# Kernel optimization log

Hardware: AMD Instinct MI355X
Metric: run time of the kernel (lower is better)

## Reference

```python
import jax, jax.numpy as jnp
import numpy as np

D_MODEL = 1024
NUM_HEADS = 16
DEPTH = D_MODEL // NUM_HEADS


def setup_inputs() -> dict:
    key = jax.random.key(0)
    k_x, k_wqkv, k_bqkv, k_wp, k_bp = jax.random.split(key, 5)
    B, N = 2, 2048
    x = jax.random.normal(k_x, (B, N, D_MODEL), dtype=jnp.float32)
    scale = 1.0 / np.sqrt(D_MODEL)
    Wqkv = jax.random.normal(k_wqkv, (D_MODEL, 3 * D_MODEL), dtype=jnp.float32) * scale
    bqkv = jnp.zeros((3 * D_MODEL,), dtype=jnp.float32)
    Wproj = jax.random.normal(k_wp, (D_MODEL, D_MODEL), dtype=jnp.float32) * scale
    bproj = jnp.zeros((D_MODEL,), dtype=jnp.float32)
    return {"x": x, "Wqkv": Wqkv, "bqkv": bqkv, "Wproj": Wproj, "bproj": bproj}


def reference(x, Wqkv, bqkv, Wproj, bproj):
    B, N, C = x.shape
    # QKV projection; original layout: [B, N, H, depth, 3] -> transpose to [B, 3, H, N, depth]
    qkv = x @ Wqkv + bqkv                      # [B, N, 3C]
    qkv = qkv.reshape(B, N, NUM_HEADS, DEPTH, 3)
    qkv = jnp.transpose(qkv, (0, 4, 2, 1, 3))  # [B, 3, H, N, depth]
    q, k, v = qkv[:, 0], qkv[:, 1], qkv[:, 2]  # each [B, H, N, depth]
    # scaled dot-product attention (full N x N scores, as in the original)
    scale = 1.0 / jnp.sqrt(jnp.asarray(DEPTH, dtype=x.dtype))
    attn = jnp.einsum("bhnd,bhmd->bhnm", q, k) * scale
    attn = jax.nn.softmax(attn.astype(jnp.float32), axis=-1).astype(x.dtype)
    out = jnp.einsum("bhnm,bhmd->bhnd", attn, v)  # [B, H, N, depth]
    out = jnp.transpose(out, (0, 2, 1, 3)).reshape(B, N, C)
    return out @ Wproj + bproj
```

## Files before the change

### kernel.cpp

```cpp
#include <hip/hip_runtime.h>
#include <stdint.h>

#define D_MODEL 1024
#define NHEADS  16
#define DEPTH   64
#define BATCH   2
#define SEQ     2048
#define M_TOK   (BATCH*SEQ)

typedef __attribute__((ext_vector_type(8)))  short short8;
typedef __attribute__((ext_vector_type(4)))  float f32x4;
typedef __attribute__((ext_vector_type(16))) float f32x16;
typedef __attribute__((ext_vector_type(4)))  unsigned int uint4v;

#if defined(__has_builtin)
#if __has_builtin(__builtin_amdgcn_exp2f)
#define EXP2(x) __builtin_amdgcn_exp2f(x)
#endif
#endif
#ifndef EXP2
#define EXP2(x) exp2f(x)
#endif

__device__ __forceinline__ unsigned short f2bf(float f) {
  unsigned int u = __float_as_uint(f);
  u += 0x7fffu + ((u >> 16) & 1u);
  return (unsigned short)(u >> 16);
}

__device__ __forceinline__ unsigned int cvt_pk_bf16(float lo, float hi) {
  unsigned int r;
  asm("v_cvt_pk_bf16_f32 %0, %1, %2" : "=v"(r) : "v"(lo), "v"(hi));
  return r;
}

__device__ __forceinline__ void gload_lds16(const unsigned short* g, unsigned short* l) {
  __builtin_amdgcn_global_load_lds((const __attribute__((address_space(1))) void*)g,
                                   (__attribute__((address_space(3))) void*)l, 16, 0, 0);
}

__global__ void mha_prep(const float* __restrict__ x, const float* __restrict__ Wqkv,
                         const float* __restrict__ Wproj,
                         unsigned short* __restrict__ xb,
                         unsigned short* __restrict__ wqkT,
                         unsigned short* __restrict__ wvT,
                         unsigned short* __restrict__ wpT) {
  __shared__ float tile[32][33];
  int id = blockIdx.x, t = threadIdx.x;
  if (id < 2048) {
    int i = (id * 256 + t) * 8;
    float4 a = *(const float4*)(x + i);
    float4 b = *(const float4*)(x + i + 4);
    uint4 r;
    r.x = (unsigned)f2bf(a.x) | ((unsigned)f2bf(a.y) << 16);
    r.y = (unsigned)f2bf(a.z) | ((unsigned)f2bf(a.w) << 16);
    r.z = (unsigned)f2bf(b.x) | ((unsigned)f2bf(b.y) << 16);
    r.w = (unsigned)f2bf(b.z) | ((unsigned)f2bf(b.w) << 16);
    *(uint4*)(xb + i) = r;
  } else if (id < 5120) {
    int b = id - 2048;
    int c0 = (b % 96) * 32, k0 = (b / 96) * 32;
    int tx = t & 31, ty = t >> 5;
    for (int i = ty; i < 32; i += 8)
      tile[i][tx] = Wqkv[(size_t)(k0 + i) * 3072 + c0 + tx];
    __syncthreads();
    for (int i = ty; i < 32; i += 8) {
      int c = c0 + i;
      int hd = c / 3;
      int s = c - hd * 3;
      unsigned short v = f2bf(tile[tx][i]);
      if (s < 2) wqkT[(size_t)(s * 1024 + hd) * 1024 + k0 + tx] = v;
      else       wvT [(size_t)hd * 1024 + k0 + tx] = v;
    }
  } else {
    int b = id - 5120;
    int c0 = (b & 31) * 32, k0 = (b >> 5) * 32;
    int tx = t & 31, ty = t >> 5;
    for (int i = ty; i < 32; i += 8)
      tile[i][tx] = Wproj[(size_t)(k0 + i) * 1024 + c0 + tx];
    __syncthreads();
    for (int i = ty; i < 32; i += 8)
      wpT[(size_t)(c0 + i) * 1024 + k0 + tx] = f2bf(tile[tx][i]);
  }
}

__global__ __launch_bounds__(256, 3) void mha_gemm_qkv(
    const unsigned short* __restrict__ xb,
    const unsigned short* __restrict__ wqkT,
    const unsigned short* __restrict__ wvT,
    const float* __restrict__ bias,
    unsigned short* __restrict__ Qb,
    unsigned short* __restrict__ Kb,
    unsigned short* __restrict__ Vtb)
{
  __shared__ __align__(16) unsigned short As[128 * 64];
  __shared__ __align__(16) unsigned short Bs[128 * 64];
  const int K = 1024;
  int id = blockIdx.x;
  bool m0 = id < 512;
  int bx, by, bz = 0;
  const unsigned short *A, *Bt;
  if (m0) {
    int xcd = id & 7, idx = id >> 3;
    by = xcd * 4 + (idx >> 4);
    bx = idx & 15;
    A = xb; Bt = wqkT;
  } else {
    int b2 = id - 512;
    bx = b2 & 15; by = (b2 >> 4) & 7; bz = b2 >> 7;
    A = wvT; Bt = xb + (size_t)bz * SEQ * D_MODEL;
  }
  int t = threadIdx.x;
  int wv = t >> 6, lane = t & 63;
  int l15 = lane & 15, l4 = lane >> 4;
  int wr = wv >> 1, wc = wv & 1;
  int blkM = by * 128, blkN = bx * 128;

  f32x4 acc[4][4];
  for (int m = 0; m < 4; m++) for (int n = 0; n < 4; n++) acc[m][n] = (f32x4){0.f,0.f,0.f,0.f};

  for (int kt = 0; kt < K; kt += 64) {
    #pragma unroll
    for (int i = 0; i < 4; i++) {
      int e = i * 256 + t;
      int row = e >> 3;
      int sc = ((e & 7) ^ (row & 7)) * 8;
      gload_lds16(A  + (size_t)(blkM + row) * K + kt + sc, As + e * 8);
      gload_lds16(Bt + (size_t)(blkN + row) * K + kt + sc, Bs + e * 8);
    }
    __syncthreads();
    #pragma unroll
    for (int kk = 0; kk < 2; kk++) {
      int gp = ((kk * 4 + l4) ^ (l15 & 7)) * 8;
      short8 af[4], bf[4];
      #pragma unroll
      for (int m = 0; m < 4; m++)
        af[m] = *(const short8*)&As[(wr * 64 + m * 16 + l15) * 64 + gp];
      #pragma unroll
      for (int n = 0; n < 4; n++)
        bf[n] = *(const short8*)&Bs[(wc * 64 + n * 16 + l15) * 64 + gp];
      #pragma unroll
      for (int m = 0; m < 4; m++)
        #pragma unroll
        for (int n = 0; n < 4; n++)
          acc[m][n] = __builtin_amdgcn_mfma_f32_16x16x32_bf16(af[m], bf[n], acc[m][n], 0, 0, 0);
    }
    __syncthreads();
  }

  int row0 = blkM + wr * 64;
  int col0 = blkN + wc * 64;
  #pragma unroll
  for (int m = 0; m < 4; m++) {
    #pragma unroll
    for (int n = 0; n < 4; n++) {
      int colb = col0 + n * 16 + l15;
      #pragma unroll
      for (int j = 0; j < 4; j++) {
        int row = row0 + m * 16 + l4 * 4 + j;
        float v = acc[m][n][j];
        if (m0) {
          int s = colb >> 10, hd = colb & 1023;
          v += bias[hd * 3 + s];
          if (s == 0) v *= 0.18033688011112042f;
          size_t idx = ((size_t)((row >> 11) * NHEADS + (hd >> 6)) * SEQ + (row & 2047)) * DEPTH + (hd & 63);
          (s == 0 ? Qb : Kb)[idx] = f2bf(v);
        } else {
          v += bias[row * 3 + 2];
          Vtb[((size_t)(bz * 1024 + row)) * SEQ + colb] = f2bf(v);
        }
      }
    }
  }
}

__global__ __launch_bounds__(256, 3) void mha_gemm_proj(
    const unsigned short* __restrict__ A,
    const unsigned short* __restrict__ Bt,
    const float* __restrict__ bias,
    float* __restrict__ out_f)
{
  __shared__ __align__(16) unsigned short As[128 * 64];
  __shared__ __align__(16) unsigned short Bs[64 * 64];
  const int K = 1024;
  int id = blockIdx.x;
  int xcd = id & 7, idx = id >> 3;
  int by = xcd * 4 + (idx >> 4);
  int bx = idx & 15;
  int t = threadIdx.x;
  int wv = t >> 6, lane = t & 63;
  int l15 = lane & 15, l4 = lane >> 4;
  int wr = wv >> 1, wc = wv & 1;
  int blkM = by * 128, blkN = bx * 64;

  f32x4 acc[4][2];
  for (int m = 0; m < 4; m++) for (int n = 0; n < 2; n++) acc[m][n] = (f32x4){0.f,0.f,0.f,0.f};

  for (int kt = 0; kt < K; kt += 64) {
    #pragma unroll
    for (int i = 0; i < 4; i++) {
      int e = i * 256 + t;
      int row = e >> 3;
      int sc = ((e & 7) ^ (row & 7)) * 8;
      gload_lds16(A + (size_t)(blkM + row) * K + kt + sc, As + e * 8);
    }
    #pragma unroll
    for (int i = 0; i < 2; i++) {
      int e = i * 256 + t;
      int row = e >> 3;
      int sc = ((e & 7) ^ (row & 7)) * 8;
      gload_lds16(Bt + (size_t)(blkN + row) * K + kt + sc, Bs + e * 8);
    }
    __syncthreads();
    #pragma unroll
    for (int kk = 0; kk < 2; kk++) {
      int gp = ((kk * 4 + l4) ^ (l15 & 7)) * 8;
      short8 af[4], bf[2];
      #pragma unroll
      for (int m = 0; m < 4; m++)
        af[m] = *(const short8*)&As[(wr * 64 + m * 16 + l15) * 64 + gp];
      #pragma unroll
      for (int n = 0; n < 2; n++)
        bf[n] = *(const short8*)&Bs[(wc * 32 + n * 16 + l15) * 64 + gp];
      #pragma unroll
      for (int m = 0; m < 4; m++)
        #pragma unroll
        for (int n = 0; n < 2; n++)
          acc[m][n] = __builtin_amdgcn_mfma_f32_16x16x32_bf16(af[m], bf[n], acc[m][n], 0, 0, 0);
    }
    __syncthreads();
  }

  int row0 = blkM + wr * 64;
  int col0 = blkN + wc * 32;
  #pragma unroll
  for (int m = 0; m < 4; m++) {
    #pragma unroll
    for (int n = 0; n < 2; n++) {
      int colb = col0 + n * 16 + l15;
      #pragma unroll
      for (int j = 0; j < 4; j++) {
        int row = row0 + m * 16 + l4 * 4 + j;
        out_f[(size_t)row * D_MODEL + colb] = acc[m][n][j] + bias[colb];
      }
    }
  }
}

__global__ __launch_bounds__(512, 2) void mha_attn(
    const unsigned short* __restrict__ Q,
    const unsigned short* __restrict__ Kb,
    const unsigned short* __restrict__ Vt,
    unsigned short* __restrict__ O)
{
  const int N = SEQ;
  const int NIT = N / 128;
  int id = blockIdx.x;
  int bh    = (id & 7) * 4 + ((id >> 7) & 3);
  int qtile = (id >> 3) & 15;
  int t = threadIdx.x, wv = t >> 6, lane = t & 63;
  int l31 = lane & 31, hi = lane >> 5;
  int kh = wv & 1, qh = wv >> 1;

  __shared__ __align__(16) unsigned short SMEM[2 * 16384];

  const unsigned short* Kbh = Kb + (size_t)bh * N * DEPTH;
  const unsigned short* Vbh = Vt + (size_t)bh * DEPTH * N;

  int qrow = qtile * 128 + qh * 32 + l31;
  const unsigned short* Qp = Q + ((size_t)bh * N + qrow) * DEPTH + hi * 8;
  short8 qf[4];
  #pragma unroll
  for (int c = 0; c < 4; c++) qf[c] = *(const short8*)(Qp + c * 16);

  int krow = t >> 3;
  int ksc  = ((t & 7) ^ (krow & 7)) * 8;
  const unsigned short* kst = Kbh + (size_t)krow * DEPTH + ksc;
  int vrow = t >> 4;
  int vg   = t & 15;
  int vsc  = ((vg ^ (vrow & 7))) * 8;
  const unsigned short* vst = Vbh + (size_t)vrow * N + vsc;

  int rbK0 = (kh * 64 + l31) * 64;
  int rbV0 = l31 * 128, rbV1 = rbV0 + 4096;
  int goQK[4], goPV[4];
  #pragma unroll
  for (int c = 0; c < 4; c++) goQK[c] = ((c * 2 + hi) ^ (l31 & 7)) * 8;
  #pragma unroll
  for (int i = 0; i < 4; i++) {
    int g = i >> 1, lc = i & 1;
    goPV[i] = ((kh * 8 + g * 4 + lc * 2 + hi) ^ (l31 & 7)) * 8;
  }

  short8 ones;
  #pragma unroll
  for (int i = 0; i < 8; i++) ones[i] = (short)0x3F80;

  f32x16 o0, o1, lsacc, zc;
  #pragma unroll
  for (int i = 0; i < 16; i++) { o0[i] = 0.f; o1[i] = 0.f; lsacc[i] = 0.f; zc[i] = 0.f; }

  gload_lds16(kst,                       SMEM + t * 8);
  gload_lds16(kst + 4096,                SMEM + 4096 + t * 8);
  gload_lds16(vst,                       SMEM + 8192 + t * 8);
  gload_lds16(vst + (size_t)32 * N,      SMEM + 12288 + t * 8);
  asm volatile("s_waitcnt vmcnt(0)" ::: "memory");
  __builtin_amdgcn_sched_barrier(0);
  __builtin_amdgcn_s_barrier();
  __builtin_amdgcn_sched_barrier(0);

#define BODY(BUF, IT)                                                                     \
  do {                                                                                    \
    if ((IT) + 1 < NIT) {                                                                 \
      unsigned short* nb = SMEM + ((BUF) ^ 1) * 16384;                                    \
      const unsigned short* kn = kst + (size_t)((IT) + 1) * 8192;                         \
      const unsigned short* vn = vst + ((IT) + 1) * 128;                                  \
      gload_lds16(kn,                  nb + t * 8);                                       \
      gload_lds16(kn + 4096,           nb + 4096 + t * 8);                                \
      gload_lds16(vn,                  nb + 8192 + t * 8);                                \
      gload_lds16(vn + (size_t)32 * N, nb + 12288 + t * 8);                               \
    }                                                                                     \
    {                                                                                     \
      const unsigned short* Kc = SMEM + (BUF) * 16384;                                    \
      const unsigned short* Vc = Kc + 8192;                                               \
      _Pragma("unroll") for (int g = 0; g < 2; g++) {                                     \
        __builtin_amdgcn_s_setprio(1);                                                    \
        short8 ka0 = *(const short8*)&Kc[rbK0 + g * 2048 + goQK[0]];                      \
        f32x16 s = __builtin_amdgcn_mfma_f32_32x32x16_bf16(ka0, qf[0], zc, 0, 0, 0);      \
        _Pragma("unroll") for (int c = 1; c < 4; c++) {                                   \
          short8 ka = *(const short8*)&Kc[rbK0 + g * 2048 + goQK[c]];                     \
          s = __builtin_amdgcn_mfma_f32_32x32x16_bf16(ka, qf[c], s, 0, 0, 0);             \
        }                                                                                 \
        __builtin_amdgcn_s_setprio(0);                                                    \
        float p[16];                                                                      \
        _Pragma("unroll") for (int r = 0; r < 16; r++) p[r] = EXP2(s[r]);                 \
        _Pragma("unroll") for (int lc = 0; lc < 2; lc++) {                                \
          unsigned int X0 = cvt_pk_bf16(p[8*lc+0], p[8*lc+1]);                            \
          unsigned int X1 = cvt_pk_bf16(p[8*lc+2], p[8*lc+3]);                            \
          unsigned int X2 = cvt_pk_bf16(p[8*lc+4], p[8*lc+5]);                            \
          unsigned int X3 = cvt_pk_bf16(p[8*lc+6], p[8*lc+7]);                            \
          auto r02 = __builtin_amdgcn_permlane32_swap(X0, X2, false, false);              \
          auto r13 = __builtin_amdgcn_permlane32_swap(X1, X3, false, false);              \
          uint4v wvec; wvec[0] = r02[0]; wvec[1] = r13[0]; wvec[2] = r02[1]; wvec[3] = r13[1]; \
          short8 bfrag = __builtin_bit_cast(short8, wvec);                                \
          short8 va = *(const short8*)&Vc[rbV0 + goPV[g * 2 + lc]];                       \
          short8 vb = *(const short8*)&Vc[rbV1 + goPV[g * 2 + lc]];                       \
          __builtin_amdgcn_s_setprio(1);                                                  \
          o0 = __builtin_amdgcn_mfma_f32_32x32x16_bf16(va, bfrag, o0, 0, 0, 0);           \
          o1 = __builtin_amdgcn_mfma_f32_32x32x16_bf16(vb, bfrag, o1, 0, 0, 0);           \
          lsacc = __builtin_amdgcn_mfma_f32_32x32x16_bf16(ones, bfrag, lsacc, 0, 0, 0);   \
          __builtin_amdgcn_s_setprio(0);                                                  \
        }                                                                                 \
      }                                                                                   \
    }                                                                                     \
    if ((IT) + 1 < NIT) {                                                                 \
      asm volatile("s_waitcnt vmcnt(0)" ::: "memory");                                    \
      __builtin_amdgcn_sched_barrier(0);                                                  \
      __builtin_amdgcn_s_barrier();                                                       \
      __builtin_amdgcn_sched_barrier(0);                                                  \
    }                                                                                     \
  } while (0)

  for (int it2 = 0; it2 < NIT; it2 += 2) {
    BODY(0, it2);
    BODY(1, it2 + 1);
  }
#undef BODY

  float ls = lsacc[0];

  __syncthreads();
  float* cmb = (float*)SMEM;
  if (kh == 1) {
    float* c0 = cmb + (qh * 64 + lane) * 33;
    #pragma unroll
    for (int i = 0; i < 16; i++) { c0[i] = o0[i]; c0[16 + i] = o1[i]; }
    c0[32] = ls;
  }
  __syncthreads();
  if (kh == 0) {
    const float* c0 = cmb + (qh * 64 + lane) * 33;
    #pragma unroll
    for (int i = 0; i < 16; i++) { o0[i] += c0[i]; o1[i] += c0[16 + i]; }
    float rl = 1.0f / (ls + c0[32]);

    int b = bh >> 4, h = bh & 15;
    unsigned short* Op = O + ((size_t)b * N + qrow) * D_MODEL + h * DEPTH;
    #pragma unroll
    for (int gq = 0; gq < 4; gq++) {
      #pragma unroll
      for (int rp = 0; rp < 2; rp++) {
        int reg = gq * 4 + rp * 2;
        int d = gq * 8 + hi * 4 + rp * 2;
        *(unsigned int*)(Op + d)      = cvt_pk_bf16(o0[reg] * rl, o0[reg + 1] * rl);
        *(unsigned int*)(Op + 32 + d) = cvt_pk_bf16(o1[reg] * rl, o1[reg + 1] * rl);
      }
    }
  }
}

extern "C" void kernel_launch(void* const* d_in, const int* in_sizes, int n_in,
                              void* d_out, int out_size, void* d_ws, size_t ws_size,
                              hipStream_t stream) {
  const float* x     = (const float*)d_in[0];
  const float* Wqkv  = (const float*)d_in[1];
  const float* bqkv  = (const float*)d_in[2];
  const float* Wproj = (const float*)d_in[3];
  const float* bproj = (const float*)d_in[4];
  float* out = (float*)d_out;

  char* w = (char*)d_ws;
  unsigned short* xb    = (unsigned short*)(w);
  unsigned short* wqkT  = (unsigned short*)(w + 8388608);
  unsigned short* wvT   = (unsigned short*)(w + 8388608 + 4194304);
  unsigned short* wpT   = (unsigned short*)(w + 8388608 + 4194304 + 2097152);
  unsigned short* Qbuf  = (unsigned short*)(w + 16777216);
  unsigned short* Kbuf  = (unsigned short*)(w + 16777216 + 8388608);
  unsigned short* Vtb   = (unsigned short*)(w + 16777216 + 16777216);
  unsigned short* AOut  = (unsigned short*)(w + 16777216 + 25165824);

  mha_prep<<<6144, 256, 0, stream>>>(x, Wqkv, Wproj, xb, wqkT, wvT, wpT);
  mha_gemm_qkv<<<768, 256, 0, stream>>>(xb, wqkT, wvT, bqkv, Qbuf, Kbuf, Vtb);
  mha_attn<<<512, 512, 0, stream>>>(Qbuf, Kbuf, Vtb, AOut);
  mha_gemm_proj<<<512, 256, 0, stream>>>(AOut, wpT, bproj, out);
}
```

Before: 110.8 us.

## Read V fragments directly from global memory and swap MFMA operand roles in PV

V tiles are no longer staged through shared memory; each wave loads its V fragments straight from global memory into registers, which halves the LDS buffer size. The PV MFMAs swap operand order so P becomes the A operand, which transposes the output layout; the row-sum accumulator now holds per-row values and is combined across waves in full. The epilogue writes scalar bf16 stores per row instead of packed pairs. This trades LDS traffic and occupancy pressure for uncoalesced, latency-exposed global loads and narrower output stores.

```diff
diff --git a/kernel.cpp b/kernel.cpp
--- a/kernel.cpp
+++ b/kernel.cpp
@@ -262,13 +262,13 @@
   int l31 = lane & 31, hi = lane >> 5;
   int kh = wv & 1, qh = wv >> 1;
 
-  __shared__ __align__(16) unsigned short SMEM[2 * 16384];
+  __shared__ __align__(16) unsigned short SMEM[25600];
 
   const unsigned short* Kbh = Kb + (size_t)bh * N * DEPTH;
   const unsigned short* Vbh = Vt + (size_t)bh * DEPTH * N;
 
-  int qrow = qtile * 128 + qh * 32 + l31;
-  const unsigned short* Qp = Q + ((size_t)bh * N + qrow) * DEPTH + hi * 8;
+  int qbase = qtile * 128 + qh * 32;
+  const unsigned short* Qp = Q + ((size_t)bh * N + qbase + l31) * DEPTH + hi * 8;
   short8 qf[4];
   #pragma unroll
   for (int c = 0; c < 4; c++) qf[c] = *(const short8*)(Qp + c * 16);
@@ -276,21 +276,14 @@
   int krow = t >> 3;
   int ksc  = ((t & 7) ^ (krow & 7)) * 8;
   const unsigned short* kst = Kbh + (size_t)krow * DEPTH + ksc;
-  int vrow = t >> 4;
-  int vg   = t & 15;
-  int vsc  = ((vg ^ (vrow & 7))) * 8;
-  const unsigned short* vst = Vbh + (size_t)vrow * N + vsc;
-
-  int rbK0 = (kh * 64 + l31) * 64;
-  int rbV0 = l31 * 128, rbV1 = rbV0 + 4096;
-  int goQK[4], goPV[4];
+
+  int rbK = (kh * 64 + l31) * 64;
+  int goQK[4];
   #pragma unroll
   for (int c = 0; c < 4; c++) goQK[c] = ((c * 2 + hi) ^ (l31 & 7)) * 8;
-  #pragma unroll
-  for (int i = 0; i < 4; i++) {
-    int g = i >> 1, lc = i & 1;
-    goPV[i] = ((kh * 8 + g * 4 + lc * 2 + hi) ^ (l31 & 7)) * 8;
-  }
+
+  const unsigned short* vb0 = Vbh + (size_t)l31 * N + kh * 64 + hi * 8;
+  const unsigned short* vb1 = vb0 + (size_t)32 * N;
 
   short8 ones;
   #pragma unroll
@@ -300,10 +293,8 @@
   #pragma unroll
   for (int i = 0; i < 16; i++) { o0[i] = 0.f; o1[i] = 0.f; lsacc[i] = 0.f; zc[i] = 0.f; }
 
-  gload_lds16(kst,                       SMEM + t * 8);
-  gload_lds16(kst + 4096,                SMEM + 4096 + t * 8);
-  gload_lds16(vst,                       SMEM + 8192 + t * 8);
-  gload_lds16(vst + (size_t)32 * N,      SMEM + 12288 + t * 8);
+  gload_lds16(kst,        SMEM + t * 8);
+  gload_lds16(kst + 4096, SMEM + 4096 + t * 8);
   asm volatile("s_waitcnt vmcnt(0)" ::: "memory");
   __builtin_amdgcn_sched_barrier(0);
   __builtin_amdgcn_s_barrier();
@@ -312,23 +303,26 @@
 #define BODY(BUF, IT)                                                                     \
   do {                                                                                    \
     if ((IT) + 1 < NIT) {                                                                 \
-      unsigned short* nb = SMEM + ((BUF) ^ 1) * 16384;                                    \
+      unsigned short* nb = SMEM + ((BUF) ^ 1) * 8192;                                     \
       const unsigned short* kn = kst + (size_t)((IT) + 1) * 8192;                         \
-      const unsigned short* vn = vst + ((IT) + 1) * 128;                                  \
-      gload_lds16(kn,                  nb + t * 8);                                       \
-      gload_lds16(kn + 4096,           nb + 4096 + t * 8);                                \
-      gload_lds16(vn,                  nb + 8192 + t * 8);                                \
-      gload_lds16(vn + (size_t)32 * N, nb + 12288 + t * 8);                               \
+      gload_lds16(kn,        nb + t * 8);                                                 \
+      gload_lds16(kn + 4096, nb + 4096 + t * 8);                                          \
     }                                                                                     \
     {                                                                                     \
-      const unsigned short* Kc = SMEM + (BUF) * 16384;                                    \
-      const unsigned short* Vc = Kc + 8192;                                               \
+      const unsigned short* Kc = SMEM + (BUF) * 8192;                                     \
+      int kt0 = (IT) * 128;                                                               \
       _Pragma("unroll") for (int g = 0; g < 2; g++) {                                     \
+                            \
+        int voff = kt0 + g * 32;                                                          \
+        short8 vf00 = *(const short8*)(vb0 + voff);                                       \
+        short8 vf01 = *(const short8*)(vb1 + voff);                                       \
+        short8 vf10 = *(const short8*)(vb0 + voff + 16);                                  \
+        short8 vf11 = *(const short8*)(vb1 + voff + 16);                                  \
         __builtin_amdgcn_s_setprio(1);                                                    \
-        short8 ka0 = *(const short8*)&Kc[rbK0 + g * 2048 + goQK[0]];                      \
+        short8 ka0 = *(const short8*)&Kc[rbK + g * 2048 + goQK[0]];                       \
         f32x16 s = __builtin_amdgcn_mfma_f32_32x32x16_bf16(ka0, qf[0], zc, 0, 0, 0);      \
         _Pragma("unroll") for (int c = 1; c < 4; c++) {                                   \
-          short8 ka = *(const short8*)&Kc[rbK0 + g * 2048 + goQK[c]];                     \
+          short8 ka = *(const short8*)&Kc[rbK + g * 2048 + goQK[c]];                      \
           s = __builtin_amdgcn_mfma_f32_32x32x16_bf16(ka, qf[c], s, 0, 0, 0);             \
         }                                                                                 \
         __builtin_amdgcn_s_setprio(0);                                                    \
@@ -342,13 +336,11 @@
           auto r02 = __builtin_amdgcn_permlane32_swap(X0, X2, false, false);              \
           auto r13 = __builtin_amdgcn_permlane32_swap(X1, X3, false, false);              \
           uint4v wvec; wvec[0] = r02[0]; wvec[1] = r13[0]; wvec[2] = r02[1]; wvec[3] = r13[1]; \
-          short8 bfrag = __builtin_bit_cast(short8, wvec);                                \
-          short8 va = *(const short8*)&Vc[rbV0 + goPV[g * 2 + lc]];                       \
-          short8 vb = *(const short8*)&Vc[rbV1 + goPV[g * 2 + lc]];                       \
+          short8 pfrag = __builtin_bit_cast(short8, wvec);                                \
           __builtin_amdgcn_s_setprio(1);                                                  \
-          o0 = __builtin_amdgcn_mfma_f32_32x32x16_bf16(va, bfrag, o0, 0, 0, 0);           \
-          o1 = __builtin_amdgcn_mfma_f32_32x32x16_bf16(vb, bfrag, o1, 0, 0, 0);           \
-          lsacc = __builtin_amdgcn_mfma_f32_32x32x16_bf16(ones, bfrag, lsacc, 0, 0, 0);   \
+          o0 = __builtin_amdgcn_mfma_f32_32x32x16_bf16(pfrag, lc ? vf10 : vf00, o0, 0, 0, 0); \
+          o1 = __builtin_amdgcn_mfma_f32_32x32x16_bf16(pfrag, lc ? vf11 : vf01, o1, 0, 0, 0); \
+          lsacc = __builtin_amdgcn_mfma_f32_32x32x16_bf16(pfrag, ones, lsacc, 0, 0, 0);   \
           __builtin_amdgcn_s_setprio(0);                                                  \
         }                                                                                 \
       }                                                                                   \
@@ -367,34 +359,28 @@
   }
 #undef BODY
 
-  float ls = lsacc[0];
-
   __syncthreads();
   float* cmb = (float*)SMEM;
   if (kh == 1) {
-    float* c0 = cmb + (qh * 64 + lane) * 33;
-    #pragma unroll
-    for (int i = 0; i < 16; i++) { c0[i] = o0[i]; c0[16 + i] = o1[i]; }
-    c0[32] = ls;
+    float* c0 = cmb + (qh * 64 + lane) * 49;
+    #pragma unroll
+    for (int i = 0; i < 16; i++) { c0[i] = o0[i]; c0[16 + i] = o1[i]; c0[32 + i] = lsacc[i]; }
   }
   __syncthreads();
   if (kh == 0) {
-    const float* c0 = cmb + (qh * 64 + lane) * 33;
-    #pragma unroll
-    for (int i = 0; i < 16; i++) { o0[i] += c0[i]; o1[i] += c0[16 + i]; }
-    float rl = 1.0f / (ls + c0[32]);
+    const float* c0 = cmb + (qh * 64 + lane) * 49;
+    #pragma unroll
+    for (int i = 0; i < 16; i++) { o0[i] += c0[i]; o1[i] += c0[16 + i]; lsacc[i] += c0[32 + i]; }
 
     int b = bh >> 4, h = bh & 15;
-    unsigned short* Op = O + ((size_t)b * N + qrow) * D_MODEL + h * DEPTH;
-    #pragma unroll
-    for (int gq = 0; gq < 4; gq++) {
-      #pragma unroll
-      for (int rp = 0; rp < 2; rp++) {
-        int reg = gq * 4 + rp * 2;
-        int d = gq * 8 + hi * 4 + rp * 2;
-        *(unsigned int*)(Op + d)      = cvt_pk_bf16(o0[reg] * rl, o0[reg + 1] * rl);
-        *(unsigned int*)(Op + 32 + d) = cvt_pk_bf16(o1[reg] * rl, o1[reg + 1] * rl);
-      }
+    unsigned short* Ob = O + ((size_t)b * N + qbase) * D_MODEL + h * DEPTH + l31;
+    #pragma unroll
+    for (int r = 0; r < 16; r++) {
+      int q = (r & 3) + 8 * (r >> 2) + 4 * hi;
+      float rl = 1.0f / lsacc[r];
+      unsigned short* Orow = Ob + (size_t)q * D_MODEL;
+      Orow[0]  = f2bf(o0[r] * rl);
+      Orow[32] = f2bf(o1[r] * rl);
     }
   }
 }
```

After: 139.4 us. +25.9%, slower.
